# Kernel optimization log

Measured on AMD Instinct MI355X. Metric: run time of the kernel, lower is better.

Reference implementation:

```python
import jax, jax.numpy as jnp
import numpy as np

# Module config (mirrors init_kwargs)
VMIN, VMAX = -1.0, 1.0
NUM_ACT_WEIGHTS = 31
INIT_SCALE = 0.04
FEATURES_OUT = 64
N, C, H, W = 8, 64, 256, 256


def setup_inputs() -> dict:
    key = jax.random.key(0)
    x = jax.random.normal(key, (N, C, H, W), dtype=jnp.float32)
    # mu: kernel centers, linspace over [vmin, vmax]
    mu = jnp.asarray(np.linspace(VMIN, VMAX, NUM_ACT_WEIGHTS, dtype=np.float32))
    # sigma: scalar std
    sigma = jnp.float32(2.0 * VMAX / (NUM_ACT_WEIGHTS - 1))
    # w: init_type 'linear' -> init_scale * x_0, repeated over feature channels
    w0 = (INIT_SCALE * np.linspace(VMIN, VMAX, NUM_ACT_WEIGHTS, dtype=np.float32))
    w0 = np.reshape(w0, (1, 1, 1, 1, NUM_ACT_WEIGHTS))
    w = jnp.asarray(np.repeat(w0, FEATURES_OUT, axis=1))  # (1,C,1,1,K)
    return {"x": x, "w": w, "mu": mu, "sigma": sigma}


def reference(x, w, mu, sigma):
    # output = sum_i w[...,i] * exp(-(x - mu_i)^2 / (2 sigma^2))
    inv_two_sig2 = 1.0 / (2.0 * sigma * sigma)
    K = w.shape[-1]
    out = jnp.zeros_like(x)
    # K is small and fixed (31); loop keeps peak memory at one NxCxHxW temp
    for i in range(K):
        d = x - mu[i]
        out = out + w[:, :, :, :, i] * jnp.exp(-(d * d) * inv_two_sig2)
    return out
```

## Files before the change

### kernel.cpp

```cpp
#include <hip/hip_runtime.h>


static constexpr int KW    = 31;
static constexpr int WIN   = 9;
static constexpr int RAD   = 4;
static constexpr int LUT_N = 1024;

typedef float f32x4 __attribute__((ext_vector_type(4)));
typedef float f32x2 __attribute__((ext_vector_type(2)));

__device__ __forceinline__ float rbf_win(float xe, const float* __restrict__ wrow,
                                         float mu0, float inv_d, float cd2, float g) {
    const float t = (xe - mu0) * inv_d;
    float jf = rintf(t) - (float)RAD;
    jf = fminf(fmaxf(jf, 0.0f), (float)(KW - WIN));
    const int s = (int)jf;
    float n = t - jf;
    n = fminf(fmaxf(n, -32.0f), 40.0f);
    float E = __builtin_amdgcn_exp2f(cd2 * n * n);
    float r = __builtin_amdgcn_exp2f(cd2 * fmaf(-2.0f, n, 1.0f));
    float acc = 0.0f;
#pragma unroll
    for (int k = 0; k < WIN; ++k) {
        acc = fmaf(wrow[s + k], E, acc);
        E *= r;
        r *= g;
    }
    return acc;
}

__global__ __launch_bounds__(256) void rbf_lut_kernel(
    const float* __restrict__ x, const float* __restrict__ w,
    const float* __restrict__ mu, const float* __restrict__ sigma,
    float* __restrict__ out, int n4, int ntot, int iters) {
    __shared__ f32x2 lut2[LUT_N];
    __shared__ float wrow[32];

    const int tid = threadIdx.x;
    const int gs  = gridDim.x * blockDim.x;
    const int gid = blockIdx.x * blockDim.x + tid;

    const int c = (gid >> 14) & 63;

    const float mu0   = mu[0];
    const float muL   = mu[KW - 1];
    const float dmu   = (muL - mu0) * (1.0f / (KW - 1));
    const float inv_d = 1.0f / dmu;
    const float sg    = sigma[0];
    const float cd2   = -1.4426950408889634f * dmu * dmu / (2.0f * sg * sg);
    const float g     = exp2f(2.0f * cd2);

    const float pad  = 5.25f * sg;
    const float lo   = mu0 - pad;
    const float span = (muL - mu0) + 2.0f * pad;
    const float h    = span * (1.0f / (float)LUT_N);
    const float invh = (float)LUT_N / span;
    const float nlo  = -lo * invh;

    int i4 = gid;
    f32x4 xv = {};
    if (i4 < n4) xv = reinterpret_cast<const f32x4*>(x)[i4];

    if (tid < KW) wrow[tid] = w[c * KW + tid];
    __syncthreads();

    for (int e = tid; e < LUT_N; e += 256) {
        const float xa = lo + (float)e * h;
        const float a  = rbf_win(xa,     wrow, mu0, inv_d, cd2, g);
        const float b  = rbf_win(xa + h, wrow, mu0, inv_d, cd2, g);
        f32x2 p; p.x = a; p.y = b - a;
        lut2[e] = p;
    }
    __syncthreads();

    const float tmax = (float)LUT_N - 0.001f;

    for (int k = 0; k < iters; ++k) {
        const int next = i4 + gs;
        f32x4 xn = xv;
        if (k + 1 < iters && next < n4) xn = reinterpret_cast<const f32x4*>(x)[next];

        if (i4 < n4) {
            f32x4 ov;
#pragma unroll
            for (int e = 0; e < 4; ++e) {
                float t = fmaf(xv[e], invh, nlo);
                t = fminf(fmaxf(t, 0.0f), tmax);
                const int j = (int)t;
                const float frac = t - (float)j;
                const f32x2 ab = lut2[j];
                ov[e] = fmaf(frac, ab.y, ab.x);
            }
            __builtin_nontemporal_store(ov, reinterpret_cast<f32x4*>(out) + i4);
        }
        xv = xn;
        i4 = next;
    }

    const float cd2x = -1.4426950408889634f / (2.0f * sg * sg);
    for (int i = n4 * 4 + gid; i < ntot; i += gs) {
        const float xe = x[i];
        const int ct = (i >> 16) & 63;
        float acc = 0.0f;
        for (int q = 0; q < KW; ++q) {
            const float d = xe - (mu0 + (float)q * dmu);
            acc = fmaf(w[ct * KW + q], __builtin_amdgcn_exp2f(cd2x * d * d), acc);
        }
        out[i] = acc;
    }
}

extern "C" void kernel_launch(void* const* d_in, const int* in_sizes, int n_in,
                              void* d_out, int out_size, void* d_ws, size_t ws_size,
                              hipStream_t stream) {
    const float* x  = (const float*)d_in[0];
    const float* w  = (const float*)d_in[1];
    const float* mu = (const float*)d_in[2];
    const float* sg = (const float*)d_in[3];
    float* out = (float*)d_out;

    const int n4     = out_size >> 2;
    const int blocks = 4096;
    const int gsz    = blocks * 256;
    const int iters  = (n4 + gsz - 1) / gsz;

    rbf_lut_kernel<<<blocks, 256, 0, stream>>>(x, w, mu, sg, out, n4, out_size, iters);
}
```

Baseline: 44.95 us.

## Specialize kernel for fixed shape with one channel per block and 16-iteration unrolled loop

Adds a shape-specialized kernel where each block owns a contiguous chunk of one channel plane (2048 blocks, 16 vec4 loads per thread, fully unrolled with prefetch), so per-block LUT construction is amortized over more elements. The LUT is changed from (value, delta) pairs to a single array of LUT_N+1 values, halving LUT build work, at the cost of two LDS reads per element instead of one 8-byte read. A generic fallback kernel is kept for other sizes.

```diff
diff --git a/kernel.cpp b/kernel.cpp
--- a/kernel.cpp
+++ b/kernel.cpp
@@ -29,19 +29,12 @@
     return acc;
 }
 
-__global__ __launch_bounds__(256) void rbf_lut_kernel(
-    const float* __restrict__ x, const float* __restrict__ w,
-    const float* __restrict__ mu, const float* __restrict__ sigma,
-    float* __restrict__ out, int n4, int ntot, int iters) {
-    __shared__ f32x2 lut2[LUT_N];
-    __shared__ float wrow[32];
-
-    const int tid = threadIdx.x;
-    const int gs  = gridDim.x * blockDim.x;
-    const int gid = blockIdx.x * blockDim.x + tid;
-
-    const int c = (gid >> 14) & 63;
-
+__device__ __forceinline__ void lut_setup(const float* __restrict__ w,
+                                          const float* __restrict__ mu,
+                                          const float* __restrict__ sigma,
+                                          int c, int tid,
+                                          float* lutA, float* wrow,
+                                          float& invh, float& nlo, float& tmax) {
     const float mu0   = mu[0];
     const float muL   = mu[KW - 1];
     const float dmu   = (muL - mu0) * (1.0f / (KW - 1));
@@ -54,57 +47,103 @@
     const float lo   = mu0 - pad;
     const float span = (muL - mu0) + 2.0f * pad;
     const float h    = span * (1.0f / (float)LUT_N);
-    const float invh = (float)LUT_N / span;
-    const float nlo  = -lo * invh;
-
-    int i4 = gid;
-    f32x4 xv = {};
-    if (i4 < n4) xv = reinterpret_cast<const f32x4*>(x)[i4];
+    invh = (float)LUT_N / span;
+    nlo  = -lo * invh;
+    tmax = (float)LUT_N - 0.001f;
 
     if (tid < KW) wrow[tid] = w[c * KW + tid];
     __syncthreads();
 
-    for (int e = tid; e < LUT_N; e += 256) {
-        const float xa = lo + (float)e * h;
-        const float a  = rbf_win(xa,     wrow, mu0, inv_d, cd2, g);
-        const float b  = rbf_win(xa + h, wrow, mu0, inv_d, cd2, g);
-        f32x2 p; p.x = a; p.y = b - a;
-        lut2[e] = p;
+    for (int e = tid; e <= LUT_N; e += 256)
+        lutA[e] = rbf_win(lo + (float)e * h, wrow, mu0, inv_d, cd2, g);
+    __syncthreads();
+}
+
+__device__ __forceinline__ float lut_eval(float xe, const float* __restrict__ lutA,
+                                          float invh, float nlo, float tmax) {
+    float t = fmaf(xe, invh, nlo);
+    t = fminf(fmaxf(t, 0.0f), tmax);
+    const int j = (int)t;
+    const float frac = t - (float)j;
+    const float a = lutA[j];
+    const float b = lutA[j + 1];
+    return fmaf(frac, b - a, a);
+}
+
+__global__ __launch_bounds__(256) void rbf_lut_fixed(
+    const float* __restrict__ x, const float* __restrict__ w,
+    const float* __restrict__ mu, const float* __restrict__ sigma,
+    float* __restrict__ out) {
+    __shared__ float lutA[LUT_N + 2];
+    __shared__ float wrow[32];
+
+    const int tid = threadIdx.x;
+    const int c   = blockIdx.x >> 5;
+    const int s   = blockIdx.x & 31;
+    const int n   = s >> 2;
+    const int q   = s & 3;
+
+    int i4 = ((n << 6) + c) * 16384 + (q << 12) + tid;
+    f32x4 xv = reinterpret_cast<const f32x4*>(x)[i4];
+
+    float invh, nlo, tmax;
+    lut_setup(w, mu, sigma, c, tid, lutA, wrow, invh, nlo, tmax);
+
+#pragma unroll
+    for (int k = 0; k < 16; ++k) {
+        f32x4 xn;
+        if (k < 15) xn = reinterpret_cast<const f32x4*>(x)[i4 + 256];
+        f32x4 ov;
+        ov.x = lut_eval(xv.x, lutA, invh, nlo, tmax);
+        ov.y = lut_eval(xv.y, lutA, invh, nlo, tmax);
+        ov.z = lut_eval(xv.z, lutA, invh, nlo, tmax);
+        ov.w = lut_eval(xv.w, lutA, invh, nlo, tmax);
+        __builtin_nontemporal_store(ov, reinterpret_cast<f32x4*>(out) + i4);
+        xv = xn;
+        i4 += 256;
     }
-    __syncthreads();
+}
 
-    const float tmax = (float)LUT_N - 0.001f;
+__global__ __launch_bounds__(256) void rbf_lut_generic(
+    const float* __restrict__ x, const float* __restrict__ w,
+    const float* __restrict__ mu, const float* __restrict__ sigma,
+    float* __restrict__ out, int n4, int ntot, int iters, int c_shift) {
+    __shared__ float lutA[LUT_N + 2];
+    __shared__ float wrow[32];
 
+    const int tid = threadIdx.x;
+    const int gs  = gridDim.x * blockDim.x;
+    const int gid = blockIdx.x * blockDim.x + tid;
+    const int c   = (gid >> c_shift) & 63;
+
+    float invh, nlo, tmax;
+    lut_setup(w, mu, sigma, c, tid, lutA, wrow, invh, nlo, tmax);
+
+    int i4 = gid;
     for (int k = 0; k < iters; ++k) {
-        const int next = i4 + gs;
-        f32x4 xn = xv;
-        if (k + 1 < iters && next < n4) xn = reinterpret_cast<const f32x4*>(x)[next];
-
         if (i4 < n4) {
+            const f32x4 xv = reinterpret_cast<const f32x4*>(x)[i4];
             f32x4 ov;
-#pragma unroll
-            for (int e = 0; e < 4; ++e) {
-                float t = fmaf(xv[e], invh, nlo);
-                t = fminf(fmaxf(t, 0.0f), tmax);
-                const int j = (int)t;
-                const float frac = t - (float)j;
-                const f32x2 ab = lut2[j];
-                ov[e] = fmaf(frac, ab.y, ab.x);
-            }
+            ov.x = lut_eval(xv.x, lutA, invh, nlo, tmax);
+            ov.y = lut_eval(xv.y, lutA, invh, nlo, tmax);
+            ov.z = lut_eval(xv.z, lutA, invh, nlo, tmax);
+            ov.w = lut_eval(xv.w, lutA, invh, nlo, tmax);
             __builtin_nontemporal_store(ov, reinterpret_cast<f32x4*>(out) + i4);
         }
-        xv = xn;
-        i4 = next;
+        i4 += gs;
     }
 
+    const float mu0 = mu[0];
+    const float dmu = (mu[KW - 1] - mu0) * (1.0f / (KW - 1));
+    const float sg  = sigma[0];
     const float cd2x = -1.4426950408889634f / (2.0f * sg * sg);
     for (int i = n4 * 4 + gid; i < ntot; i += gs) {
         const float xe = x[i];
-        const int ct = (i >> 16) & 63;
+        const int ct = (i >> (c_shift + 2)) & 63;
         float acc = 0.0f;
-        for (int q = 0; q < KW; ++q) {
-            const float d = xe - (mu0 + (float)q * dmu);
-            acc = fmaf(w[ct * KW + q], __builtin_amdgcn_exp2f(cd2x * d * d), acc);
+        for (int qq = 0; qq < KW; ++qq) {
+            const float d = xe - (mu0 + (float)qq * dmu);
+            acc = fmaf(w[ct * KW + qq], __builtin_amdgcn_exp2f(cd2x * d * d), acc);
         }
         out[i] = acc;
     }
@@ -119,10 +158,14 @@
     const float* sg = (const float*)d_in[3];
     float* out = (float*)d_out;
 
-    const int n4     = out_size >> 2;
-    const int blocks = 4096;
-    const int gsz    = blocks * 256;
-    const int iters  = (n4 + gsz - 1) / gsz;
-
-    rbf_lut_kernel<<<blocks, 256, 0, stream>>>(x, w, mu, sg, out, n4, out_size, iters);
+    if (out_size == 8 * 64 * 65536) {
+        rbf_lut_fixed<<<2048, 256, 0, stream>>>(x, w, mu, sg, out);
+    } else {
+        const int n4     = out_size >> 2;
+        const int blocks = 4096;
+        const int gsz    = blocks * 256;
+        const int iters  = (n4 + gsz - 1) / gsz;
+        rbf_lut_generic<<<blocks, 256, 0, stream>>>(x, w, mu, sg, out, n4, out_size,
+                                                    iters, 14);
+    }
 }
```

Result: no change. 45.77 us (+1.8%).
